# Kernel tuning notes

Hardware: AMD Instinct MI355X
Metric: run time of the kernel (lower is better)

Reference implementation:

```python
import jax, jax.numpy as jnp
import numpy as np

IN_DIMS = (8, 8, 8, 8)
OUT_DIMS = (8, 8, 8, 8)
RANKS = (1, 16, 16, 16, 1)
BATCH = 4096


def setup_inputs() -> dict:
    key = jax.random.key(0)
    ks = jax.random.split(key, 6)
    n_in = int(np.prod(IN_DIMS))
    n_out = int(np.prod(OUT_DIMS))
    d = len(IN_DIMS)
    # t3f glorot: total matrix variance 2/(n_in+n_out), split evenly across cores/ranks
    lamb = 2.0 / (n_in + n_out)
    cv = (lamb / np.prod(RANKS)) ** (1.0 / d)
    core_std = float(np.sqrt(cv))
    cores = {}
    for i in range(d):
        shp = (RANKS[i], IN_DIMS[i], OUT_DIMS[i], RANKS[i + 1])
        cores[f"core{i}"] = core_std * jax.random.normal(ks[i], shp, dtype=jnp.float32)
    x = jax.random.normal(ks[4], (BATCH, n_in), dtype=jnp.float32)
    b = 0.1 * jnp.ones((n_out,), dtype=jnp.float32)
    return {"x": x, **cores, "b": b}


def tt_dense(x, cores):
    """y = x @ M, M the TT-matrix with cores [r_{k-1}, a_k, b_k, r_k]."""
    B = x.shape[0]
    rest = int(np.prod(IN_DIMS[1:]))
    # t: [B, P(out dims done), r, a_k, rest(in dims todo)]
    t = x.reshape(B, 1, 1, IN_DIMS[0], rest)
    for k, core in enumerate(cores):
        # contract rank r and input mode a_k -> produce output mode b_k and next rank q
        t = jnp.einsum('zpras,rabq->zpbqs', t, core)
        z, p, bd, q, s = t.shape
        if k < len(cores) - 1:
            a_next = IN_DIMS[k + 1]
            t = t.reshape(z, p * bd, q, a_next, s // a_next)
        else:
            t = t.reshape(z, p * bd)  # q == s == 1
    return t  # [B, prod(OUT_DIMS)]


def reference(x, core0, core1, core2, core3, b):
    y = tt_dense(x, [core0, core1, core2, core3])
    return jax.nn.relu(y + b)
```

## Files before the change

kernel.cpp:

```cpp
#include <hip/hip_runtime.h>
#include <hip/hip_bf16.h>
#include <cstdint>
#include <cstddef>


#define GM 4096
#define GN 4096
#define GK 4096

typedef __attribute__((ext_vector_type(8))) short short8_t;
typedef __attribute__((ext_vector_type(4))) float float4_t;

__device__ __forceinline__ unsigned short f2bf(float f) {
  union { float f; uint32_t u; } v; v.f = f;
  uint32_t u = v.u;
  uint32_t r = (u + 0x7fffu + ((u >> 16) & 1u)) >> 16;
  return (unsigned short)r;
}

__global__ __launch_bounds__(256) void prep_convert(
    const float* __restrict__ c0, const float* __restrict__ c1,
    const float* __restrict__ c2, const float* __restrict__ c3,
    float* __restrict__ G01, float* __restrict__ G23t,
    const float* __restrict__ x, unsigned short* __restrict__ xb) {
  int bid = blockIdx.x;
  if (bid < 512) {
    int idx = bid * 256 + threadIdx.x;
    if (idx < 65536) {
      int r2 = idx & 15;
      int b01 = (idx >> 4) & 63;
      int a01 = idx >> 10;
      int a0 = a01 >> 3, a1 = a01 & 7, b0 = b01 >> 3, b1 = b01 & 7;
      float s = 0.f;
#pragma unroll
      for (int r1 = 0; r1 < 16; ++r1)
        s += c0[(a0 * 8 + b0) * 16 + r1] * c1[((r1 * 8 + a1) * 8 + b1) * 16 + r2];
      G01[idx] = s;
    } else {
      int t = idx - 65536;
      int a23 = t & 63;
      int b23 = (t >> 6) & 63;
      int r2 = t >> 12;
      int a2 = a23 >> 3, a3 = a23 & 7, b2 = b23 >> 3, b3 = b23 & 7;
      float s = 0.f;
#pragma unroll
      for (int r3 = 0; r3 < 16; ++r3)
        s += c2[((r2 * 8 + a2) * 8 + b2) * 16 + r3] * c3[(r3 * 8 + a3) * 8 + b3];
      G23t[t] = s;
    }
  } else {
    int i = ((bid - 512) * 256 + threadIdx.x) * 8;
    float4_t a = *(const float4_t*)(x + i);
    float4_t b = *(const float4_t*)(x + i + 4);
    short8_t o;
    o[0] = (short)f2bf(a[0]); o[1] = (short)f2bf(a[1]);
    o[2] = (short)f2bf(a[2]); o[3] = (short)f2bf(a[3]);
    o[4] = (short)f2bf(b[0]); o[5] = (short)f2bf(b[1]);
    o[6] = (short)f2bf(b[2]); o[7] = (short)f2bf(b[3]);
    *(short8_t*)(xb + i) = o;
  }
}

__global__ __launch_bounds__(256) void build_mt(
    const float* __restrict__ G01, const float* __restrict__ G23t,
    unsigned short* __restrict__ Mt) {
  int a01 = blockIdx.x >> 4;
  int g = blockIdx.x & 15;
  int tid = threadIdx.x;

  float acc[4][16];
#pragma unroll
  for (int j = 0; j < 4; ++j)
#pragma unroll
    for (int i = 0; i < 16; ++i) acc[j][i] = 0.f;

  for (int r2 = 0; r2 < 16; ++r2) {
    float gv[4];
#pragma unroll
    for (int j = 0; j < 4; ++j)
      gv[j] = G01[(a01 * 64 + g * 4 + j) * 16 + r2];
    const float* src = G23t + r2 * 4096 + tid * 16;
    float4_t v0 = *(const float4_t*)(src);
    float4_t v1 = *(const float4_t*)(src + 4);
    float4_t v2 = *(const float4_t*)(src + 8);
    float4_t v3 = *(const float4_t*)(src + 12);
#pragma unroll
    for (int j = 0; j < 4; ++j) {
#pragma unroll
      for (int l = 0; l < 4; ++l) {
        acc[j][l]      += gv[j] * v0[l];
        acc[j][4 + l]  += gv[j] * v1[l];
        acc[j][8 + l]  += gv[j] * v2[l];
        acc[j][12 + l] += gv[j] * v3[l];
      }
    }
  }

  int b23 = tid >> 2;
  int a23base = (tid & 3) * 16;
#pragma unroll
  for (int j = 0; j < 4; ++j) {
    short8_t o0, o1;
#pragma unroll
    for (int i = 0; i < 8; ++i) {
      o0[i] = (short)f2bf(acc[j][i]);
      o1[i] = (short)f2bf(acc[j][8 + i]);
    }
    size_t base = (size_t)((g * 4 + j) * 64 + b23) * GK + a01 * 64 + a23base;
    *(short8_t*)(Mt + base) = o0;
    *(short8_t*)(Mt + base + 8) = o1;
  }
}

__global__ __launch_bounds__(256) void gemm_bias_relu(
    const unsigned short* __restrict__ A, const unsigned short* __restrict__ Bt,
    const float* __restrict__ bias, float* __restrict__ C) {
  __shared__ __align__(16) unsigned short As[128 * 64];
  __shared__ __align__(16) unsigned short Bs[128 * 64];

  int tid = threadIdx.x;
  int row0 = (int)(blockIdx.x >> 5) * 128;
  int col0 = (int)(blockIdx.x & 31) * 128;
  int wave = tid >> 6, lane = tid & 63;
  int wr = (wave >> 1) * 64, wc = (wave & 1) * 64;
  int half = lane >> 4, mrow = lane & 15;

  float4_t acc[4][4];
#pragma unroll
  for (int i = 0; i < 4; ++i)
#pragma unroll
    for (int j = 0; j < 4; ++j) acc[i][j] = (float4_t){0.f, 0.f, 0.f, 0.f};

  const unsigned short* Ap[4];
  const unsigned short* Bp[4];
  int cdst[4];
#pragma unroll
  for (int q = 0; q < 4; ++q) {
    int c = q * 256 + tid;
    int r = c >> 3;
    int h = ((c & 7) - (r >> 1)) & 7;
    Ap[q] = A + (size_t)(row0 + r) * GK + h * 8;
    Bp[q] = Bt + (size_t)(col0 + r) * GK + h * 8;
    cdst[q] = c * 8;
  }

  int aoff[2][4], boff[2][4];
#pragma unroll
  for (int ks = 0; ks < 2; ++ks) {
#pragma unroll
    for (int i = 0; i < 4; ++i) {
      int rA = wr + i * 16 + mrow;
      aoff[ks][i] = rA * 64 + ((((ks * 4 + half) + (rA >> 1)) & 7) * 8);
      int rB = wc + i * 16 + mrow;
      boff[ks][i] = rB * 64 + ((((ks * 4 + half) + (rB >> 1)) & 7) * 8);
    }
  }

  for (int k0 = 0; k0 < GK; k0 += 64) {
#pragma unroll
    for (int q = 0; q < 4; ++q) {
      __builtin_amdgcn_global_load_lds(
          (const __attribute__((address_space(1))) void*)(Ap[q] + k0),
          (__attribute__((address_space(3))) void*)(As + cdst[q]), 16, 0, 0);
      __builtin_amdgcn_global_load_lds(
          (const __attribute__((address_space(1))) void*)(Bp[q] + k0),
          (__attribute__((address_space(3))) void*)(Bs + cdst[q]), 16, 0, 0);
    }
    __syncthreads();

#pragma unroll
    for (int ks = 0; ks < 2; ++ks) {
      short8_t af[4], bfr[4];
#pragma unroll
      for (int i = 0; i < 4; ++i) af[i] = *(const short8_t*)&As[aoff[ks][i]];
#pragma unroll
      for (int j = 0; j < 4; ++j) bfr[j] = *(const short8_t*)&Bs[boff[ks][j]];
#pragma unroll
      for (int i = 0; i < 4; ++i)
#pragma unroll
        for (int j = 0; j < 4; ++j)
          acc[i][j] = __builtin_amdgcn_mfma_f32_16x16x32_bf16(af[i], bfr[j],
                                                              acc[i][j], 0, 0, 0);
    }
    __syncthreads();
  }

#pragma unroll
  for (int j = 0; j < 4; ++j) {
    int col = col0 + wc + j * 16 + mrow;
    float bcol = bias[col];
#pragma unroll
    for (int i = 0; i < 4; ++i) {
#pragma unroll
      for (int r = 0; r < 4; ++r) {
        int row = row0 + wr + i * 16 + half * 4 + r;
        float v = acc[i][j][r] + bcol;
        C[(size_t)row * GN + col] = v > 0.f ? v : 0.f;
      }
    }
  }
}

extern "C" void kernel_launch(void* const* d_in, const int* in_sizes, int n_in,
                              void* d_out, int out_size, void* d_ws, size_t ws_size,
                              hipStream_t stream) {
  const float* x  = (const float*)d_in[0];
  const float* c0 = (const float*)d_in[1];
  const float* c1 = (const float*)d_in[2];
  const float* c2 = (const float*)d_in[3];
  const float* c3 = (const float*)d_in[4];
  const float* b  = (const float*)d_in[5];
  float* out = (float*)d_out;

  unsigned short* xb = (unsigned short*)d_ws;
  unsigned short* Mt = (unsigned short*)((char*)d_ws + (32u << 20));
  float* G01 = (float*)((char*)d_ws + (64u << 20));
  float* G23t = G01 + 65536;

  prep_convert<<<512 + (GM * GK) / (256 * 8), 256, 0, stream>>>(
      c0, c1, c2, c3, G01, G23t, x, xb);
  build_mt<<<1024, 256, 0, stream>>>(G01, G23t, Mt);
  gemm_bias_relu<<<(GM / 128) * (GN / 128), 256, 0, stream>>>(xb, Mt, b, out);
}
```

Measured before the change: 282.1 us.

## Fuse TT core contraction into one pre-kernel, swizzle GEMM tiles per XCD

Merges the G01/G23 partial contractions and the dense TT-matrix build into a single kernel. Each block recomputes its small G slices in shared memory and writes one row of Mt, and the same launch also converts x to bf16. This removes one launch and the global round trip for the intermediate G buffers, at the cost of redundant recomputation of the core products per block. The GEMM also remaps block indices so each XCD works on a contiguous region for L2 locality, and changes the LDS XOR swizzle from row/2 to row.

```diff
diff --git a/kernel.cpp b/kernel.cpp
--- a/kernel.cpp
+++ b/kernel.cpp
@@ -7,6 +7,9 @@
 #define GM 4096
 #define GN 4096
 #define GK 4096
+
+#define MT_BLOCKS 4096
+#define CONV_BLOCKS 8192
 
 typedef __attribute__((ext_vector_type(8))) short short8_t;
 typedef __attribute__((ext_vector_type(4))) float float4_t;
@@ -18,38 +21,75 @@
   return (unsigned short)r;
 }
 
-__global__ __launch_bounds__(256) void prep_convert(
+__global__ __launch_bounds__(256) void pre_kernel(
     const float* __restrict__ c0, const float* __restrict__ c1,
     const float* __restrict__ c2, const float* __restrict__ c3,
-    float* __restrict__ G01, float* __restrict__ G23t,
-    const float* __restrict__ x, unsigned short* __restrict__ xb) {
+    const float* __restrict__ x, unsigned short* __restrict__ xb,
+    unsigned short* __restrict__ Mt) {
   int bid = blockIdx.x;
-  if (bid < 512) {
-    int idx = bid * 256 + threadIdx.x;
-    if (idx < 65536) {
-      int r2 = idx & 15;
-      int b01 = (idx >> 4) & 63;
-      int a01 = idx >> 10;
-      int a0 = a01 >> 3, a1 = a01 & 7, b0 = b01 >> 3, b1 = b01 & 7;
-      float s = 0.f;
-#pragma unroll
-      for (int r1 = 0; r1 < 16; ++r1)
-        s += c0[(a0 * 8 + b0) * 16 + r1] * c1[((r1 * 8 + a1) * 8 + b1) * 16 + r2];
-      G01[idx] = s;
-    } else {
-      int t = idx - 65536;
-      int a23 = t & 63;
-      int b23 = (t >> 6) & 63;
-      int r2 = t >> 12;
-      int a2 = a23 >> 3, a3 = a23 & 7, b2 = b23 >> 3, b3 = b23 & 7;
-      float s = 0.f;
-#pragma unroll
-      for (int r3 = 0; r3 < 16; ++r3)
-        s += c2[((r2 * 8 + a2) * 8 + b2) * 16 + r3] * c3[(r3 * 8 + a3) * 8 + b3];
-      G23t[t] = s;
-    }
+  if (bid < MT_BLOCKS) {
+    __shared__ float G01s[16 * 64];
+    __shared__ float G23s[16 * 64];
+    int b01 = bid >> 6, b23 = bid & 63;
+    int b0 = b01 >> 3, b1 = b01 & 7, b2 = b23 >> 3, b3 = b23 & 7;
+    int tid = threadIdx.x;
+#pragma unroll
+    for (int u = 0; u < 4; ++u) {
+      int e = tid * 4 + u;
+      {
+        int a01 = e >> 4, r2 = e & 15;
+        int a0 = a01 >> 3, a1 = a01 & 7;
+        float s = 0.f;
+#pragma unroll
+        for (int r1 = 0; r1 < 16; ++r1)
+          s += c0[(a0 * 8 + b0) * 16 + r1] *
+               c1[((r1 * 8 + a1) * 8 + b1) * 16 + r2];
+        G01s[r2 * 64 + a01] = s;
+      }
+      {
+        int r2 = e >> 6, a23 = e & 63;
+        int a2 = a23 >> 3, a3 = a23 & 7;
+        float s = 0.f;
+#pragma unroll
+        for (int r3 = 0; r3 < 16; ++r3)
+          s += c2[((r2 * 8 + a2) * 8 + b2) * 16 + r3] *
+               c3[(r3 * 8 + a3) * 8 + b3];
+        G23s[r2 * 64 + a23] = s;
+      }
+    }
+    __syncthreads();
+
+    int a01 = tid >> 2;
+    int a23b = (tid & 3) * 16;
+    float acc[16];
+#pragma unroll
+    for (int i = 0; i < 16; ++i) acc[i] = 0.f;
+    for (int r2 = 0; r2 < 16; ++r2) {
+      float g = G01s[r2 * 64 + a01];
+      const float* row = &G23s[r2 * 64 + a23b];
+      float4_t v0 = *(const float4_t*)(row);
+      float4_t v1 = *(const float4_t*)(row + 4);
+      float4_t v2 = *(const float4_t*)(row + 8);
+      float4_t v3 = *(const float4_t*)(row + 12);
+#pragma unroll
+      for (int l = 0; l < 4; ++l) {
+        acc[l]      += g * v0[l];
+        acc[4 + l]  += g * v1[l];
+        acc[8 + l]  += g * v2[l];
+        acc[12 + l] += g * v3[l];
+      }
+    }
+    short8_t o0, o1;
+#pragma unroll
+    for (int i = 0; i < 8; ++i) {
+      o0[i] = (short)f2bf(acc[i]);
+      o1[i] = (short)f2bf(acc[8 + i]);
+    }
+    size_t base = (size_t)bid * GK + tid * 16;
+    *(short8_t*)(Mt + base) = o0;
+    *(short8_t*)(Mt + base + 8) = o1;
   } else {
-    int i = ((bid - 512) * 256 + threadIdx.x) * 8;
+    int i = ((bid - MT_BLOCKS) * 256 + threadIdx.x) * 8;
     float4_t a = *(const float4_t*)(x + i);
     float4_t b = *(const float4_t*)(x + i + 4);
     short8_t o;
@@ -61,57 +101,6 @@
   }
 }
 
-__global__ __launch_bounds__(256) void build_mt(
-    const float* __restrict__ G01, const float* __restrict__ G23t,
-    unsigned short* __restrict__ Mt) {
-  int a01 = blockIdx.x >> 4;
-  int g = blockIdx.x & 15;
-  int tid = threadIdx.x;
-
-  float acc[4][16];
-#pragma unroll
-  for (int j = 0; j < 4; ++j)
-#pragma unroll
-    for (int i = 0; i < 16; ++i) acc[j][i] = 0.f;
-
-  for (int r2 = 0; r2 < 16; ++r2) {
-    float gv[4];
-#pragma unroll
-    for (int j = 0; j < 4; ++j)
-      gv[j] = G01[(a01 * 64 + g * 4 + j) * 16 + r2];
-    const float* src = G23t + r2 * 4096 + tid * 16;
-    float4_t v0 = *(const float4_t*)(src);
-    float4_t v1 = *(const float4_t*)(src + 4);
-    float4_t v2 = *(const float4_t*)(src + 8);
-    float4_t v3 = *(const float4_t*)(src + 12);
-#pragma unroll
-    for (int j = 0; j < 4; ++j) {
-#pragma unroll
-      for (int l = 0; l < 4; ++l) {
-        acc[j][l]      += gv[j] * v0[l];
-        acc[j][4 + l]  += gv[j] * v1[l];
-        acc[j][8 + l]  += gv[j] * v2[l];
-        acc[j][12 + l] += gv[j] * v3[l];
-      }
-    }
-  }
-
-  int b23 = tid >> 2;
-  int a23base = (tid & 3) * 16;
-#pragma unroll
-  for (int j = 0; j < 4; ++j) {
-    short8_t o0, o1;
-#pragma unroll
-    for (int i = 0; i < 8; ++i) {
-      o0[i] = (short)f2bf(acc[j][i]);
-      o1[i] = (short)f2bf(acc[j][8 + i]);
-    }
-    size_t base = (size_t)((g * 4 + j) * 64 + b23) * GK + a01 * 64 + a23base;
-    *(short8_t*)(Mt + base) = o0;
-    *(short8_t*)(Mt + base + 8) = o1;
-  }
-}
-
 __global__ __launch_bounds__(256) void gemm_bias_relu(
     const unsigned short* __restrict__ A, const unsigned short* __restrict__ Bt,
     const float* __restrict__ bias, float* __restrict__ C) {
@@ -119,8 +108,10 @@
   __shared__ __align__(16) unsigned short Bs[128 * 64];
 
   int tid = threadIdx.x;
-  int row0 = (int)(blockIdx.x >> 5) * 128;
-  int col0 = (int)(blockIdx.x & 31) * 128;
+  int bswz = blockIdx.x;
+  int xcd = bswz & 7, li = bswz >> 3;
+  int row0 = (((xcd >> 1) * 8) + (li >> 4)) * 128;
+  int col0 = (((xcd & 1) * 16) + (li & 15)) * 128;
   int wave = tid >> 6, lane = tid & 63;
   int wr = (wave >> 1) * 64, wc = (wave & 1) * 64;
   int half = lane >> 4, mrow = lane & 15;
@@ -138,7 +129,7 @@
   for (int q = 0; q < 4; ++q) {
     int c = q * 256 + tid;
     int r = c >> 3;
-    int h = ((c & 7) - (r >> 1)) & 7;
+    int h = ((c & 7) - r) & 7;
     Ap[q] = A + (size_t)(row0 + r) * GK + h * 8;
     Bp[q] = Bt + (size_t)(col0 + r) * GK + h * 8;
     cdst[q] = c * 8;
@@ -150,9 +141,9 @@
 #pragma unroll
     for (int i = 0; i < 4; ++i) {
       int rA = wr + i * 16 + mrow;
-      aoff[ks][i] = rA * 64 + ((((ks * 4 + half) + (rA >> 1)) & 7) * 8);
+      aoff[ks][i] = rA * 64 + ((((ks * 4 + half) + rA) & 7) * 8);
       int rB = wc + i * 16 + mrow;
-      boff[ks][i] = rB * 64 + ((((ks * 4 + half) + (rB >> 1)) & 7) * 8);
+      boff[ks][i] = rB * 64 + ((((ks * 4 + half) + rB) & 7) * 8);
     }
   }
 
@@ -214,11 +205,8 @@
 
   unsigned short* xb = (unsigned short*)d_ws;
   unsigned short* Mt = (unsigned short*)((char*)d_ws + (32u << 20));
-  float* G01 = (float*)((char*)d_ws + (64u << 20));
-  float* G23t = G01 + 65536;
-
-  prep_convert<<<512 + (GM * GK) / (256 * 8), 256, 0, stream>>>(
-      c0, c1, c2, c3, G01, G23t, x, xb);
-  build_mt<<<1024, 256, 0, stream>>>(G01, G23t, Mt);
+
+  pre_kernel<<<MT_BLOCKS + CONV_BLOCKS, 256, 0, stream>>>(
+      c0, c1, c2, c3, x, xb, Mt);
   gemm_bias_relu<<<(GM / 128) * (GN / 128), 256, 0, stream>>>(xb, Mt, b, out);
 }
```

Measured after the change: 345.2 us. 1.22x slower.

## Load GEMM fragments directly from global memory and swizzle blocks per XCD

Applied to the files above, without the earlier changes.

Removes the LDS staging and barriers from the bf16 GEMM. Each wave now loads its MFMA fragments straight from global memory into registers. Block indices are also remapped so blocks on the same XCD cover a contiguous region of the output, to improve L2 reuse. The trade-off is that operand reuse across the waves of a block now depends on caches rather than shared memory, which raises global/L1 traffic, and each 16-byte row-strided load has no prefetch overlap.

```diff
diff --git a/kernel.cpp b/kernel.cpp
--- a/kernel.cpp
+++ b/kernel.cpp
@@ -115,12 +115,11 @@
 __global__ __launch_bounds__(256) void gemm_bias_relu(
     const unsigned short* __restrict__ A, const unsigned short* __restrict__ Bt,
     const float* __restrict__ bias, float* __restrict__ C) {
-  __shared__ __align__(16) unsigned short As[128 * 64];
-  __shared__ __align__(16) unsigned short Bs[128 * 64];
-
   int tid = threadIdx.x;
-  int row0 = (int)(blockIdx.x >> 5) * 128;
-  int col0 = (int)(blockIdx.x & 31) * 128;
+  int bswz = blockIdx.x;
+  int xcd = bswz & 7, li = bswz >> 3;
+  int row0 = (((xcd >> 1) * 8) + (li >> 4)) * 128;
+  int col0 = (((xcd & 1) * 16) + (li & 15)) * 128;
   int wave = tid >> 6, lane = tid & 63;
   int wr = (wave >> 1) * 64, wc = (wave & 1) * 64;
   int half = lane >> 4, mrow = lane & 15;
@@ -131,58 +130,33 @@
 #pragma unroll
     for (int j = 0; j < 4; ++j) acc[i][j] = (float4_t){0.f, 0.f, 0.f, 0.f};
 
-  const unsigned short* Ap[4];
-  const unsigned short* Bp[4];
-  int cdst[4];
+  const short8_t* Ap[4];
+  const short8_t* Bp[4];
 #pragma unroll
-  for (int q = 0; q < 4; ++q) {
-    int c = q * 256 + tid;
-    int r = c >> 3;
-    int h = ((c & 7) - (r >> 1)) & 7;
-    Ap[q] = A + (size_t)(row0 + r) * GK + h * 8;
-    Bp[q] = Bt + (size_t)(col0 + r) * GK + h * 8;
-    cdst[q] = c * 8;
+  for (int i = 0; i < 4; ++i) {
+    Ap[i] = (const short8_t*)(A + (size_t)(row0 + wr + i * 16 + mrow) * GK +
+                              half * 8);
+    Bp[i] = (const short8_t*)(Bt + (size_t)(col0 + wc + i * 16 + mrow) * GK +
+                              half * 8);
   }
 
-  int aoff[2][4], boff[2][4];
+  for (int k8 = 0; k8 < GK / 8; k8 += 8) {
+    short8_t af[2][4], bfr[2][4];
 #pragma unroll
-  for (int ks = 0; ks < 2; ++ks) {
+    for (int ks = 0; ks < 2; ++ks)
 #pragma unroll
-    for (int i = 0; i < 4; ++i) {
-      int rA = wr + i * 16 + mrow;
-      aoff[ks][i] = rA * 64 + ((((ks * 4 + half) + (rA >> 1)) & 7) * 8);
-      int rB = wc + i * 16 + mrow;
-      boff[ks][i] = rB * 64 + ((((ks * 4 + half) + (rB >> 1)) & 7) * 8);
-    }
-  }
-
-  for (int k0 = 0; k0 < GK; k0 += 64) {
+      for (int i = 0; i < 4; ++i) {
+        af[ks][i] = Ap[i][k8 + ks * 4];
+        bfr[ks][i] = Bp[i][k8 + ks * 4];
+      }
 #pragma unroll
-    for (int q = 0; q < 4; ++q) {
-      __builtin_amdgcn_global_load_lds(
-          (const __attribute__((address_space(1))) void*)(Ap[q] + k0),
-          (__attribute__((address_space(3))) void*)(As + cdst[q]), 16, 0, 0);
-      __builtin_amdgcn_global_load_lds(
-          (const __attribute__((address_space(1))) void*)(Bp[q] + k0),
-          (__attribute__((address_space(3))) void*)(Bs + cdst[q]), 16, 0, 0);
-    }
-    __syncthreads();
-
-#pragma unroll
-    for (int ks = 0; ks < 2; ++ks) {
-      short8_t af[4], bfr[4];
-#pragma unroll
-      for (int i = 0; i < 4; ++i) af[i] = *(const short8_t*)&As[aoff[ks][i]];
-#pragma unroll
-      for (int j = 0; j < 4; ++j) bfr[j] = *(const short8_t*)&Bs[boff[ks][j]];
+    for (int ks = 0; ks < 2; ++ks)
 #pragma unroll
       for (int i = 0; i < 4; ++i)
 #pragma unroll
         for (int j = 0; j < 4; ++j)
-          acc[i][j] = __builtin_amdgcn_mfma_f32_16x16x32_bf16(af[i], bfr[j],
-                                                              acc[i][j], 0, 0, 0);
-    }
-    __syncthreads();
+          acc[i][j] = __builtin_amdgcn_mfma_f32_16x16x32_bf16(
+              af[ks][i], bfr[ks][j], acc[i][j], 0, 0, 0);
   }
 
 #pragma unroll
```

New measurement: 618.8 us. 2.19x slower.

## Rebalance prep kernels, add XCD-aware block mapping and change LDS swizzle

Applied to the files above, without the earlier changes.

Moves the x-to-bf16 conversion out of the small core-contraction kernel and into the Mt-building kernel. The tiny G01/G23 prep now runs alone and the large conversion work overlaps the Mt construction. The GEMM remaps block indices so that each of the 8 XCDs owns a contiguous 8x16 tile region, which should improve L2 reuse of A and B. The LDS XOR swizzle changes from row/2 to row to cut bank conflicts on the fragment reads.

```diff
diff --git a/kernel.cpp b/kernel.cpp
--- a/kernel.cpp
+++ b/kernel.cpp
@@ -18,38 +18,89 @@
   return (unsigned short)r;
 }
 
-__global__ __launch_bounds__(256) void prep_convert(
+__global__ __launch_bounds__(256) void prep_kernel(
     const float* __restrict__ c0, const float* __restrict__ c1,
     const float* __restrict__ c2, const float* __restrict__ c3,
-    float* __restrict__ G01, float* __restrict__ G23t,
+    float* __restrict__ G01, float* __restrict__ G23t) {
+  int idx = blockIdx.x * 256 + threadIdx.x;
+  if (idx < 65536) {
+    int r2 = idx & 15;
+    int b01 = (idx >> 4) & 63;
+    int a01 = idx >> 10;
+    int a0 = a01 >> 3, a1 = a01 & 7, b0 = b01 >> 3, b1 = b01 & 7;
+    float s = 0.f;
+#pragma unroll
+    for (int r1 = 0; r1 < 16; ++r1)
+      s += c0[(a0 * 8 + b0) * 16 + r1] * c1[((r1 * 8 + a1) * 8 + b1) * 16 + r2];
+    G01[idx] = s;
+  } else {
+    int t = idx - 65536;
+    int a23 = t & 63;
+    int b23 = (t >> 6) & 63;
+    int r2 = t >> 12;
+    int a2 = a23 >> 3, a3 = a23 & 7, b2 = b23 >> 3, b3 = b23 & 7;
+    float s = 0.f;
+#pragma unroll
+    for (int r3 = 0; r3 < 16; ++r3)
+      s += c2[((r2 * 8 + a2) * 8 + b2) * 16 + r3] * c3[(r3 * 8 + a3) * 8 + b3];
+    G23t[t] = s;
+  }
+}
+
+__global__ __launch_bounds__(256) void mt_convert(
+    const float* __restrict__ G01, const float* __restrict__ G23t,
+    unsigned short* __restrict__ Mt,
     const float* __restrict__ x, unsigned short* __restrict__ xb) {
   int bid = blockIdx.x;
-  if (bid < 512) {
-    int idx = bid * 256 + threadIdx.x;
-    if (idx < 65536) {
-      int r2 = idx & 15;
-      int b01 = (idx >> 4) & 63;
-      int a01 = idx >> 10;
-      int a0 = a01 >> 3, a1 = a01 & 7, b0 = b01 >> 3, b1 = b01 & 7;
-      float s = 0.f;
-#pragma unroll
-      for (int r1 = 0; r1 < 16; ++r1)
-        s += c0[(a0 * 8 + b0) * 16 + r1] * c1[((r1 * 8 + a1) * 8 + b1) * 16 + r2];
-      G01[idx] = s;
-    } else {
-      int t = idx - 65536;
-      int a23 = t & 63;
-      int b23 = (t >> 6) & 63;
-      int r2 = t >> 12;
-      int a2 = a23 >> 3, a3 = a23 & 7, b2 = b23 >> 3, b3 = b23 & 7;
-      float s = 0.f;
-#pragma unroll
-      for (int r3 = 0; r3 < 16; ++r3)
-        s += c2[((r2 * 8 + a2) * 8 + b2) * 16 + r3] * c3[(r3 * 8 + a3) * 8 + b3];
-      G23t[t] = s;
+  int tid = threadIdx.x;
+  if (bid < 1024) {
+    int a01 = bid >> 4;
+    int g = bid & 15;
+
+    float acc[4][16];
+#pragma unroll
+    for (int j = 0; j < 4; ++j)
+#pragma unroll
+      for (int i = 0; i < 16; ++i) acc[j][i] = 0.f;
+
+    for (int r2 = 0; r2 < 16; ++r2) {
+      float gv[4];
+#pragma unroll
+      for (int j = 0; j < 4; ++j)
+        gv[j] = G01[(a01 * 64 + g * 4 + j) * 16 + r2];
+      const float* src = G23t + r2 * 4096 + tid * 16;
+      float4_t v0 = *(const float4_t*)(src);
+      float4_t v1 = *(const float4_t*)(src + 4);
+      float4_t v2 = *(const float4_t*)(src + 8);
+      float4_t v3 = *(const float4_t*)(src + 12);
+#pragma unroll
+      for (int j = 0; j < 4; ++j) {
+#pragma unroll
+        for (int l = 0; l < 4; ++l) {
+          acc[j][l]      += gv[j] * v0[l];
+          acc[j][4 + l]  += gv[j] * v1[l];
+          acc[j][8 + l]  += gv[j] * v2[l];
+          acc[j][12 + l] += gv[j] * v3[l];
+        }
+      }
+    }
+
+    int b23 = tid >> 2;
+    int a23base = (tid & 3) * 16;
+#pragma unroll
+    for (int j = 0; j < 4; ++j) {
+      short8_t o0, o1;
+#pragma unroll
+      for (int i = 0; i < 8; ++i) {
+        o0[i] = (short)f2bf(acc[j][i]);
+        o1[i] = (short)f2bf(acc[j][8 + i]);
+      }
+      size_t base = (size_t)((g * 4 + j) * 64 + b23) * GK + a01 * 64 + a23base;
+      *(short8_t*)(Mt + base) = o0;
+      *(short8_t*)(Mt + base + 8) = o1;
     }
   } else {
-    int i = ((bid - 512) * 256 + threadIdx.x) * 8;
+    int i = ((bid - 1024) * 256 + tid) * 8;
     float4_t a = *(const float4_t*)(x + i);
     float4_t b = *(const float4_t*)(x + i + 4);
     short8_t o;
@@ -61,57 +112,6 @@
   }
 }
 
-__global__ __launch_bounds__(256) void build_mt(
-    const float* __restrict__ G01, const float* __restrict__ G23t,
-    unsigned short* __restrict__ Mt) {
-  int a01 = blockIdx.x >> 4;
-  int g = blockIdx.x & 15;
-  int tid = threadIdx.x;
-
-  float acc[4][16];
-#pragma unroll
-  for (int j = 0; j < 4; ++j)
-#pragma unroll
-    for (int i = 0; i < 16; ++i) acc[j][i] = 0.f;
-
-  for (int r2 = 0; r2 < 16; ++r2) {
-    float gv[4];
-#pragma unroll
-    for (int j = 0; j < 4; ++j)
-      gv[j] = G01[(a01 * 64 + g * 4 + j) * 16 + r2];
-    const float* src = G23t + r2 * 4096 + tid * 16;
-    float4_t v0 = *(const float4_t*)(src);
-    float4_t v1 = *(const float4_t*)(src + 4);
-    float4_t v2 = *(const float4_t*)(src + 8);
-    float4_t v3 = *(const float4_t*)(src + 12);
-#pragma unroll
-    for (int j = 0; j < 4; ++j) {
-#pragma unroll
-      for (int l = 0; l < 4; ++l) {
-        acc[j][l]      += gv[j] * v0[l];
-        acc[j][4 + l]  += gv[j] * v1[l];
-        acc[j][8 + l]  += gv[j] * v2[l];
-        acc[j][12 + l] += gv[j] * v3[l];
-      }
-    }
-  }
-
-  int b23 = tid >> 2;
-  int a23base = (tid & 3) * 16;
-#pragma unroll
-  for (int j = 0; j < 4; ++j) {
-    short8_t o0, o1;
-#pragma unroll
-    for (int i = 0; i < 8; ++i) {
-      o0[i] = (short)f2bf(acc[j][i]);
-      o1[i] = (short)f2bf(acc[j][8 + i]);
-    }
-    size_t base = (size_t)((g * 4 + j) * 64 + b23) * GK + a01 * 64 + a23base;
-    *(short8_t*)(Mt + base) = o0;
-    *(short8_t*)(Mt + base + 8) = o1;
-  }
-}
-
 __global__ __launch_bounds__(256) void gemm_bias_relu(
     const unsigned short* __restrict__ A, const unsigned short* __restrict__ Bt,
     const float* __restrict__ bias, float* __restrict__ C) {
@@ -119,8 +119,10 @@
   __shared__ __align__(16) unsigned short Bs[128 * 64];
 
   int tid = threadIdx.x;
-  int row0 = (int)(blockIdx.x >> 5) * 128;
-  int col0 = (int)(blockIdx.x & 31) * 128;
+  int bswz = blockIdx.x;
+  int xcd = bswz & 7, li = bswz >> 3;
+  int row0 = (((xcd >> 1) * 8) + (li >> 4)) * 128;
+  int col0 = (((xcd & 1) * 16) + (li & 15)) * 128;
   int wave = tid >> 6, lane = tid & 63;
   int wr = (wave >> 1) * 64, wc = (wave & 1) * 64;
   int half = lane >> 4, mrow = lane & 15;
@@ -138,7 +140,7 @@
   for (int q = 0; q < 4; ++q) {
     int c = q * 256 + tid;
     int r = c >> 3;
-    int h = ((c & 7) - (r >> 1)) & 7;
+    int h = ((c & 7) - r) & 7;
     Ap[q] = A + (size_t)(row0 + r) * GK + h * 8;
     Bp[q] = Bt + (size_t)(col0 + r) * GK + h * 8;
     cdst[q] = c * 8;
@@ -150,9 +152,9 @@
 #pragma unroll
     for (int i = 0; i < 4; ++i) {
       int rA = wr + i * 16 + mrow;
-      aoff[ks][i] = rA * 64 + ((((ks * 4 + half) + (rA >> 1)) & 7) * 8);
+      aoff[ks][i] = rA * 64 + ((((ks * 4 + half) + rA) & 7) * 8);
       int rB = wc + i * 16 + mrow;
-      boff[ks][i] = rB * 64 + ((((ks * 4 + half) + (rB >> 1)) & 7) * 8);
+      boff[ks][i] = rB * 64 + ((((ks * 4 + half) + rB) & 7) * 8);
     }
   }
 
@@ -217,8 +219,8 @@
   float* G01 = (float*)((char*)d_ws + (64u << 20));
   float* G23t = G01 + 65536;
 
-  prep_convert<<<512 + (GM * GK) / (256 * 8), 256, 0, stream>>>(
-      c0, c1, c2, c3, G01, G23t, x, xb);
-  build_mt<<<1024, 256, 0, stream>>>(G01, G23t, Mt);
+  prep_kernel<<<512, 256, 0, stream>>>(c0, c1, c2, c3, G01, G23t);
+  mt_convert<<<1024 + (GM * GK) / (256 * 8), 256, 0, stream>>>(
+      G01, G23t, Mt, x, xb);
   gemm_bias_relu<<<(GM / 128) * (GN / 128), 256, 0, stream>>>(xb, Mt, b, out);
 }
```

Result: faster. 268.7 us (-4.8%).
